# Performance work log

Hardware: AMD Instinct MI355X
Metric: run time of the kernel (lower is better)

Reference implementation:

```python
import jax, jax.numpy as jnp
import numpy as np

RHO = 1.0
EPSILON = 0.1
N_ITERS = 5
EPS = 1e-08


def setup_inputs() -> dict:
    key = jax.random.key(0)
    k1, k2, k3 = jax.random.split(key, 3)
    B, H, M, N, D = 16, 16, 256, 576, 1024
    # student cross-attention weights: positive, rows roughly sum to 1 (post-softmax in the real model)
    sa = jax.random.uniform(k1, (B, H, M, N), dtype=jnp.float32) + 1e-3
    student_attn = sa / sa.sum(axis=-1, keepdims=True)
    visual_feats = jax.random.normal(k2, (B, N, D), dtype=jnp.float32)
    text_feats = jax.random.normal(k3, (B, M, D), dtype=jnp.float32)
    text_mask = jnp.ones((B, M), dtype=jnp.float32)
    return {"student_attn": student_attn, "visual_feats": visual_feats,
            "text_feats": text_feats, "text_mask": text_mask}


def _l2norm(x):
    return x / jnp.sqrt(jnp.sum(x * x, axis=-1, keepdims=True) + 1e-12)


def _teacher_plan(x, y, y_mask):
    # x: (B,N,D) visual, y: (B,M,D) text, y_mask: (B,M)
    B, N, D = x.shape
    M = y.shape[1]
    x_n = _l2norm(x)
    y_n = _l2norm(y)
    cost = 1.0 - jnp.einsum('bmd,bnd->bmn', y_n, x_n)          # (B,M,N)
    mu = jnp.full((B, N, 1), 1.0 / N, dtype=x.dtype)            # visual marginal (column vec)
    nu = (y_mask / (jnp.sum(y_mask, axis=1, keepdims=True) + EPS))[:, :, None]  # (B,M,1)
    K = jnp.exp(-cost / EPSILON)                                # (B,M,N)
    fi = RHO / (RHO + EPSILON)
    u = jnp.ones((B, M, 1), dtype=x.dtype)
    v = jnp.ones((B, N, 1), dtype=x.dtype)
    for _ in range(N_ITERS):
        Kv = jnp.einsum('bmn,bnk->bmk', K, v)                   # (B,M,1)
        u = (nu / (Kv + EPS)) ** fi
        Ktu = jnp.einsum('bmn,bmk->bnk', K, u)                  # (B,N,1)
        v = (mu / (Ktu + EPS)) ** fi
    P = u * K * jnp.swapaxes(v, 1, 2)                           # (B,M,N)
    return P / (jnp.sum(P, axis=-1, keepdims=True) + EPS)


def reference(student_attn, visual_feats, text_feats, text_mask):
    teacher = jax.lax.stop_gradient(_teacher_plan(visual_feats, text_feats, text_mask))
    teacher = teacher[:, None, :, :]                            # (B,1,M,N)
    loss = -jnp.sum(teacher * jnp.log(student_attn + EPS), axis=-1)  # (B,H,M)
    loss = loss * text_mask[:, None, :]
    return jnp.mean(loss)
```

## Files before the change

kernel.cpp:

```cpp
#include <hip/hip_runtime.h>
#include <math.h>

#define B_ 16
#define H_ 16
#define M_ 256
#define N_ 576
#define D_ 1024
#define BK 64
#define LDS_STRIDE (BK + 8)
#define NROWS (B_ * N_ + B_ * M_)

constexpr float EPS_ = 1e-8f;
constexpr float FI_ = 0.90909090909090906f;

typedef __bf16 bf16x8 __attribute__((ext_vector_type(8)));
typedef float f32x4 __attribute__((ext_vector_type(4)));

__device__ __forceinline__ float wave_reduce(float v) {
#pragma unroll
  for (int o = 32; o > 0; o >>= 1) v += __shfl_down(v, o, 64);
  return v;
}

__device__ __forceinline__ unsigned short f2bf(float f) {
  union { float f; unsigned u; } a; a.f = f;
  unsigned r = a.u + 0x7fff + ((a.u >> 16) & 1);
  return (unsigned short)(r >> 16);
}

__device__ __forceinline__ float bf2f(unsigned short u) {
  union { unsigned u; float f; } a; a.u = ((unsigned)u) << 16;
  return a.f;
}

__global__ __launch_bounds__(256) void prep_kernel(const float* __restrict__ vis,
                                                   const float* __restrict__ txt,
                                                   const float* __restrict__ mask,
                                                   unsigned short* __restrict__ xb,
                                                   unsigned short* __restrict__ yb,
                                                   float* __restrict__ masksum) {
  const int bid = blockIdx.x;
  const int lane = threadIdx.x & 63;
  if (bid < NROWS / 4) {
    int wave = bid * 4 + (threadIdx.x >> 6);
    const float* src;
    unsigned short* dst;
    if (wave < B_ * N_) {
      src = vis + (size_t)wave * D_;
      dst = xb + (size_t)wave * D_;
    } else {
      int r = wave - B_ * N_;
      src = txt + (size_t)r * D_;
      dst = yb + (size_t)r * D_;
    }
    float4 v[4];
    float s = 0.f;
#pragma unroll
    for (int it = 0; it < 4; ++it) {
      v[it] = *(const float4*)&src[it * 256 + lane * 4];
      s += v[it].x * v[it].x + v[it].y * v[it].y + v[it].z * v[it].z + v[it].w * v[it].w;
    }
    s = wave_reduce(s);
    s = __shfl(s, 0, 64);
    float inv = rsqrtf(s + 1e-12f);
#pragma unroll
    for (int it = 0; it < 4; ++it) {
      ushort4 pk;
      pk.x = f2bf(v[it].x * inv);
      pk.y = f2bf(v[it].y * inv);
      pk.z = f2bf(v[it].z * inv);
      pk.w = f2bf(v[it].w * inv);
      *(ushort4*)&dst[it * 256 + lane * 4] = pk;
    }
  } else {
    int b = (bid - NROWS / 4) * 4 + (threadIdx.x >> 6);
    float4 mv = *(const float4*)&mask[b * M_ + lane * 4];
    float s = wave_reduce(mv.x + mv.y + mv.z + mv.w);
    if (lane == 0) masksum[b] = s;
  }
}

__global__ __launch_bounds__(256) void gemm_k_mfma(const unsigned short* __restrict__ xb,
                                                   const unsigned short* __restrict__ yb,
                                                   unsigned short* __restrict__ Kw) {
  __shared__ unsigned short As[64][LDS_STRIDE];
  __shared__ unsigned short Bs[64][LDS_STRIDE];
  const int b = blockIdx.z;
  const int m0 = blockIdx.y * 64;
  const int n0 = blockIdx.x * 64;
  const unsigned short* Y = yb + (size_t)b * M_ * D_;
  const unsigned short* X = xb + (size_t)b * N_ * D_;
  const int t = threadIdx.x;
  const int lane = t & 63;
  const int w = t >> 6;
  const int wm = (w & 1) * 32;
  const int wn = (w >> 1) * 32;
  const int lr = t >> 3;
  const int lc = (t & 7) * 8;
  const int fr = lane & 15;
  const int fk = (lane >> 4) * 8;

  f32x4 acc[2][2] = {};
  for (int k0 = 0; k0 < D_; k0 += BK) {
#pragma unroll
    for (int p = 0; p < 2; ++p) {
      *(uint4*)&As[lr + 32 * p][lc] = *(const uint4*)&Y[(size_t)(m0 + lr + 32 * p) * D_ + k0 + lc];
      *(uint4*)&Bs[lr + 32 * p][lc] = *(const uint4*)&X[(size_t)(n0 + lr + 32 * p) * D_ + k0 + lc];
    }
    __syncthreads();
#pragma unroll
    for (int ks = 0; ks < BK; ks += 32) {
      bf16x8 a[2], bfr[2];
#pragma unroll
      for (int i = 0; i < 2; ++i) {
        a[i] = *(const bf16x8*)&As[wm + i * 16 + fr][ks + fk];
        bfr[i] = *(const bf16x8*)&Bs[wn + i * 16 + fr][ks + fk];
      }
#pragma unroll
      for (int i = 0; i < 2; ++i)
#pragma unroll
        for (int j = 0; j < 2; ++j)
          acc[i][j] = __builtin_amdgcn_mfma_f32_16x16x32_bf16(a[i], bfr[j], acc[i][j], 0, 0, 0);
    }
    __syncthreads();
  }

  const int cm = (lane >> 4) * 4;
  const int cn = lane & 15;
#pragma unroll
  for (int i = 0; i < 2; ++i)
#pragma unroll
    for (int j = 0; j < 2; ++j)
#pragma unroll
      for (int rg = 0; rg < 4; ++rg) {
        int m = m0 + wm + i * 16 + cm + rg;
        int n = n0 + wn + j * 16 + cn;
        Kw[((size_t)b * M_ + m) * N_ + n] = f2bf(expf(10.f * (acc[i][j][rg] - 1.f)));
      }
}


__global__ __launch_bounds__(256) void sink_u_first(const unsigned short* __restrict__ Kw,
                                                    const float* __restrict__ mask,
                                                    const float* __restrict__ masksum,
                                                    float* __restrict__ u) {
  const int b = blockIdx.y;
  const int row = blockIdx.x * 4 + (threadIdx.x >> 6);
  const int lane = threadIdx.x & 63;
  const unsigned short* rowp = Kw + ((size_t)b * M_ + row) * N_;
  float s = 0.f;
#pragma unroll
  for (int k = 0; k < 9; ++k) s += bf2f(rowp[lane + 64 * k]);
  s = wave_reduce(s);
  if (lane == 0) {
    int idx = b * M_ + row;
    float nu = mask[idx] / (masksum[b] + EPS_);
    u[idx] = powf(nu / (s + EPS_), FI_);
  }
}

__global__ __launch_bounds__(256) void sink_u(const unsigned short* __restrict__ Kw,
                                              const float* __restrict__ v,
                                              const float* __restrict__ mask,
                                              const float* __restrict__ masksum,
                                              float* __restrict__ u) {
  const int b = blockIdx.y;
  const int row = blockIdx.x * 4 + (threadIdx.x >> 6);
  const int lane = threadIdx.x & 63;
  const unsigned short* rowp = Kw + ((size_t)b * M_ + row) * N_;
  const float* vb = v + b * N_;
  float s = 0.f;
#pragma unroll
  for (int k = 0; k < 9; ++k) s += bf2f(rowp[lane + 64 * k]) * vb[lane + 64 * k];
  s = wave_reduce(s);
  if (lane == 0) {
    int idx = b * M_ + row;
    float nu = mask[idx] / (masksum[b] + EPS_);
    u[idx] = powf(nu / (s + EPS_), FI_);
  }
}

__global__ __launch_bounds__(256) void sink_v(const unsigned short* __restrict__ Kw,
                                              const float* __restrict__ u,
                                              float* __restrict__ v) {
  __shared__ float part[4][64];
  const int b = blockIdx.y;
  const int n0 = blockIdx.x * 64;
  const int col = n0 + (threadIdx.x & 63);
  const int g = threadIdx.x >> 6;
  const unsigned short* Kb = Kw + (size_t)b * M_ * N_;
  const float* ub = u + b * M_;
  float s = 0.f;
#pragma unroll 8
  for (int m = g * 64; m < (g + 1) * 64; ++m) s += bf2f(Kb[(size_t)m * N_ + col]) * ub[m];
  part[g][threadIdx.x & 63] = s;
  __syncthreads();
  if (threadIdx.x < 64) {
    float tot = part[0][threadIdx.x] + part[1][threadIdx.x] +
                part[2][threadIdx.x] + part[3][threadIdx.x];
    v[b * N_ + n0 + threadIdx.x] = powf((1.f / (float)N_) / (tot + EPS_), FI_);
  }
}

__global__ __launch_bounds__(256) void loss_fused(const float* __restrict__ student,
                                                  const unsigned short* __restrict__ Kw,
                                                  const float* __restrict__ v,
                                                  const float* __restrict__ mask,
                                                  float* __restrict__ out) {
  __shared__ float kv[N_];
  __shared__ float red[4];
  __shared__ float sh_scale;
  const int m = blockIdx.x;
  const int b = blockIdx.y;
  const int t = threadIdx.x;

  const unsigned short* rowp = Kw + ((size_t)b * M_ + m) * N_;
  const float* vb = v + b * N_;
  float part = 0.f;
  for (int i = t; i < N_; i += 256) {
    float val = bf2f(rowp[i]) * vb[i];
    kv[i] = val;
    part += val;
  }
  part = wave_reduce(part);
  if ((t & 63) == 0) red[t >> 6] = part;
  __syncthreads();
  if (t == 0) {
    float Kv = red[0] + red[1] + red[2] + red[3];
    sh_scale = mask[b * M_ + m] / (Kv + EPS_);
  }

  const float* st = student + ((size_t)b * H_ * M_ + m) * N_;
  float acc = 0.f;
#pragma unroll 1
  for (int i = t; i < H_ * (N_ / 4); i += 256) {
    int h = i / (N_ / 4);
    int n4 = i - h * (N_ / 4);
    float4 s4 = *(const float4*)&st[(size_t)h * M_ * N_ + n4 * 4];
    float4 k4 = *(const float4*)&kv[n4 * 4];
    acc -= k4.x * __logf(s4.x + EPS_) + k4.y * __logf(s4.y + EPS_) +
           k4.z * __logf(s4.z + EPS_) + k4.w * __logf(s4.w + EPS_);
  }
  acc = wave_reduce(acc);
  __syncthreads();
  if ((t & 63) == 0) red[t >> 6] = acc;
  __syncthreads();
  if (t == 0) {
    float tot = red[0] + red[1] + red[2] + red[3];
    atomicAdd(out, sh_scale * tot * (1.f / ((float)B_ * H_ * M_)));
  }
}

extern "C" void kernel_launch(void* const* d_in, const int* in_sizes, int n_in,
                              void* d_out, int out_size, void* d_ws, size_t ws_size,
                              hipStream_t stream) {
  const float* student = (const float*)d_in[0];
  const float* vis = (const float*)d_in[1];
  const float* txt = (const float*)d_in[2];
  const float* mask = (const float*)d_in[3];
  float* out = (float*)d_out;

  char* p = (char*)d_ws;
  unsigned short* Kb = (unsigned short*)p; p += (size_t)B_ * M_ * N_ * 2;
  unsigned short* xb = (unsigned short*)p; p += (size_t)B_ * N_ * D_ * 2;
  unsigned short* yb = (unsigned short*)p; p += (size_t)B_ * M_ * D_ * 2;
  float* vv = (float*)p;      p += B_ * N_ * 4;
  float* uu = (float*)p;      p += B_ * M_ * 4;
  float* msum = (float*)p;    p += B_ * 4;

  hipMemsetAsync(d_out, 0, sizeof(float), stream);
  prep_kernel<<<NROWS / 4 + 4, 256, 0, stream>>>(vis, txt, mask, xb, yb, msum);
  gemm_k_mfma<<<dim3(N_ / 64, M_ / 64, B_), 256, 0, stream>>>(xb, yb, Kb);

  sink_u_first<<<dim3(M_ / 4, B_), 256, 0, stream>>>(Kb, mask, msum, uu);
  sink_v<<<dim3(N_ / 64, B_), 256, 0, stream>>>(Kb, uu, vv);
  for (int it = 1; it < 5; ++it) {
    sink_u<<<dim3(M_ / 4, B_), 256, 0, stream>>>(Kb, vv, mask, msum, uu);
    sink_v<<<dim3(N_ / 64, B_), 256, 0, stream>>>(Kb, uu, vv);
  }

  loss_fused<<<dim3(M_, B_), 256, 0, stream>>>(student, Kb, vv, mask, out);
}
```

Measured before the change: 353.0 us.

## Precompute head-summed log student attention, split loss into separate passes

Since the teacher weights do not depend on the head index, the log of student attention is summed over heads in a separate kernel that streams the student tensor once and writes a (B,M,N) sum. The final loss kernel then needs only K, v and that sum, which removes per-head multiplies by the plan. The atomicAdd and memset are replaced by a per-row partial buffer and a single-block reduction. In exchange this adds a 9.4 MB intermediate write plus a read, and two extra kernel launches. The sumlog pass also uses only 144 of 256 threads per block.

Measured after the change: 335.6 us. -4.9%, faster.

```diff
diff --git a/kernel.cpp b/kernel.cpp
--- a/kernel.cpp
+++ b/kernel.cpp
@@ -31,6 +31,25 @@
 __device__ __forceinline__ float bf2f(unsigned short u) {
   union { unsigned u; float f; } a; a.u = ((unsigned)u) << 16;
   return a.f;
+}
+
+__global__ __launch_bounds__(256) void sumlog_kernel(const float* __restrict__ student,
+                                                     float* __restrict__ SL) {
+  const int m = blockIdx.x;
+  const int b = blockIdx.y;
+  const int t = threadIdx.x;
+  if (t >= N_ / 4) return;
+  const float* st = student + ((size_t)b * H_ * M_ + m) * N_ + t * 4;
+  float4 acc = {0.f, 0.f, 0.f, 0.f};
+#pragma unroll
+  for (int h = 0; h < H_; ++h) {
+    float4 s4 = *(const float4*)&st[(size_t)h * M_ * N_];
+    acc.x += __logf(s4.x + EPS_);
+    acc.y += __logf(s4.y + EPS_);
+    acc.z += __logf(s4.z + EPS_);
+    acc.w += __logf(s4.w + EPS_);
+  }
+  *(float4*)&SL[((size_t)b * M_ + m) * N_ + t * 4] = acc;
 }
 
 __global__ __launch_bounds__(256) void prep_kernel(const float* __restrict__ vis,
@@ -202,53 +221,47 @@
   }
 }
 
-__global__ __launch_bounds__(256) void loss_fused(const float* __restrict__ student,
-                                                  const unsigned short* __restrict__ Kw,
-                                                  const float* __restrict__ v,
-                                                  const float* __restrict__ mask,
-                                                  float* __restrict__ out) {
-  __shared__ float kv[N_];
-  __shared__ float red[4];
-  __shared__ float sh_scale;
+__global__ __launch_bounds__(256) void finloss_kernel(const unsigned short* __restrict__ Kw,
+                                                      const float* __restrict__ SL,
+                                                      const float* __restrict__ v,
+                                                      const float* __restrict__ mask,
+                                                      float* __restrict__ partial) {
+  __shared__ float red[2][4];
   const int m = blockIdx.x;
   const int b = blockIdx.y;
   const int t = threadIdx.x;
-
-  const unsigned short* rowp = Kw + ((size_t)b * M_ + m) * N_;
-  const float* vb = v + b * N_;
-  float part = 0.f;
-  for (int i = t; i < N_; i += 256) {
-    float val = bf2f(rowp[i]) * vb[i];
-    kv[i] = val;
-    part += val;
-  }
-  part = wave_reduce(part);
-  if ((t & 63) == 0) red[t >> 6] = part;
+  float s1 = 0.f, s2 = 0.f;
+  if (t < N_ / 4) {
+    const unsigned short* kp = Kw + ((size_t)b * M_ + m) * N_ + t * 4;
+    ushort4 k4 = *(const ushort4*)kp;
+    float4 v4 = *(const float4*)&v[b * N_ + t * 4];
+    float4 sl4 = *(const float4*)&SL[((size_t)b * M_ + m) * N_ + t * 4];
+    float kv0 = bf2f(k4.x) * v4.x, kv1 = bf2f(k4.y) * v4.y;
+    float kv2 = bf2f(k4.z) * v4.z, kv3 = bf2f(k4.w) * v4.w;
+    s1 = kv0 + kv1 + kv2 + kv3;
+    s2 = kv0 * sl4.x + kv1 * sl4.y + kv2 * sl4.z + kv3 * sl4.w;
+  }
+  s1 = wave_reduce(s1);
+  s2 = wave_reduce(s2);
+  if ((t & 63) == 0) { red[0][t >> 6] = s1; red[1][t >> 6] = s2; }
   __syncthreads();
   if (t == 0) {
-    float Kv = red[0] + red[1] + red[2] + red[3];
-    sh_scale = mask[b * M_ + m] / (Kv + EPS_);
-  }
-
-  const float* st = student + ((size_t)b * H_ * M_ + m) * N_;
-  float acc = 0.f;
-#pragma unroll 1
-  for (int i = t; i < H_ * (N_ / 4); i += 256) {
-    int h = i / (N_ / 4);
-    int n4 = i - h * (N_ / 4);
-    float4 s4 = *(const float4*)&st[(size_t)h * M_ * N_ + n4 * 4];
-    float4 k4 = *(const float4*)&kv[n4 * 4];
-    acc -= k4.x * __logf(s4.x + EPS_) + k4.y * __logf(s4.y + EPS_) +
-           k4.z * __logf(s4.z + EPS_) + k4.w * __logf(s4.w + EPS_);
-  }
-  acc = wave_reduce(acc);
+    float S1 = red[0][0] + red[0][1] + red[0][2] + red[0][3];
+    float S2 = red[1][0] + red[1][1] + red[1][2] + red[1][3];
+    int row = b * M_ + m;
+    partial[row] = -mask[row] * S2 / ((S1 + EPS_) * (float)(B_ * H_ * M_));
+  }
+}
+
+__global__ __launch_bounds__(256) void reduce_kernel(const float* __restrict__ partial,
+                                                     float* __restrict__ out) {
+  __shared__ float red[4];
+  float s = 0.f;
+  for (int i = threadIdx.x; i < B_ * M_; i += 256) s += partial[i];
+  s = wave_reduce(s);
+  if ((threadIdx.x & 63) == 0) red[threadIdx.x >> 6] = s;
   __syncthreads();
-  if ((t & 63) == 0) red[t >> 6] = acc;
-  __syncthreads();
-  if (t == 0) {
-    float tot = red[0] + red[1] + red[2] + red[3];
-    atomicAdd(out, sh_scale * tot * (1.f / ((float)B_ * H_ * M_)));
-  }
+  if (threadIdx.x == 0) out[0] = red[0] + red[1] + red[2] + red[3];
 }
 
 extern "C" void kernel_launch(void* const* d_in, const int* in_sizes, int n_in,
@@ -264,11 +277,14 @@
   unsigned short* Kb = (unsigned short*)p; p += (size_t)B_ * M_ * N_ * 2;
   unsigned short* xb = (unsigned short*)p; p += (size_t)B_ * N_ * D_ * 2;
   unsigned short* yb = (unsigned short*)p; p += (size_t)B_ * M_ * D_ * 2;
+  float* SL = (float*)p;      p += (size_t)B_ * M_ * N_ * 4;
   float* vv = (float*)p;      p += B_ * N_ * 4;
   float* uu = (float*)p;      p += B_ * M_ * 4;
   float* msum = (float*)p;    p += B_ * 4;
-
-  hipMemsetAsync(d_out, 0, sizeof(float), stream);
+  float* partial = (float*)p; p += B_ * M_ * 4;
+
+  sumlog_kernel<<<dim3(M_, B_), 256, 0, stream>>>(student, SL);
+
   prep_kernel<<<NROWS / 4 + 4, 256, 0, stream>>>(vis, txt, mask, xb, yb, msum);
   gemm_k_mfma<<<dim3(N_ / 64, M_ / 64, B_), 256, 0, stream>>>(xb, yb, Kb);
 
@@ -279,5 +295,6 @@
     sink_v<<<dim3(N_ / 64, B_), 256, 0, stream>>>(Kb, uu, vv);
   }
 
-  loss_fused<<<dim3(M_, B_), 256, 0, stream>>>(student, Kb, vv, mask, out);
-}
+  finloss_kernel<<<dim3(M_, B_), 256, 0, stream>>>(Kb, SL, vv, mask, partial);
+  reduce_kernel<<<1, 256, 0, stream>>>(partial, out);
+}
```
